# Kernel optimization log

Hardware: AMD Instinct MI355X
Metric: run time of the kernel (lower is better)

## Reference

```python
import jax, jax.numpy as jnp
import numpy as np
import math

IN_DIM = 256
HID_DIM = 256
NUM_EDGE_TYPES = 3
HEADS = 8
HEAD_DIM = HID_DIM // HEADS  # 32
QK_DIM = (NUM_EDGE_TYPES + 1) * HID_DIM  # 1024
N = 4096


def _glorot(key, shape):
    # torch_geometric-style glorot: uniform(-a, a), a = sqrt(6/(fan_in+fan_out)) over last two dims
    a = math.sqrt(6.0 / (shape[-2] + shape[-1]))
    return jax.random.uniform(key, shape, jnp.float32, -a, a)


def setup_inputs() -> dict:
    key = jax.random.key(0)
    ks = jax.random.split(key, 8)
    return {
        "input_x": jax.random.normal(ks[0], (N, IN_DIM), jnp.float32),
        "pe_Q": jax.random.normal(ks[1], (N, NUM_EDGE_TYPES * HID_DIM), jnp.float32),
        "pe_K": jax.random.normal(ks[2], (N, NUM_EDGE_TYPES * HID_DIM), jnp.float32),
        "A": jnp.zeros((N, N), jnp.int32),  # accepted by forward but unused
        "WQ": _glorot(ks[3], (HEADS, QK_DIM, HEAD_DIM)),
        "WK": _glorot(ks[4], (HEADS, QK_DIM, HEAD_DIM)),
        "WV": _glorot(ks[5], (HEADS, IN_DIM, HEAD_DIM)),
        "Q_bias": jnp.zeros((HEADS, 1, HEAD_DIM), jnp.float32),
        "K_bias": jnp.zeros((HEADS, 1, HEAD_DIM), jnp.float32),
        "V_bias": jnp.zeros((HEADS, 1, HEAD_DIM), jnp.float32),
        "lin_w": _glorot(ks[6], (HID_DIM, HID_DIM)),
        "lin_b": jnp.zeros((HID_DIM,), jnp.float32),
    }


def reference(input_x, pe_Q, pe_K, A, WQ, WK, WV, Q_bias, K_bias, V_bias, lin_w, lin_b):
    x_Q = jnp.concatenate([input_x, pe_Q], axis=-1)  # [N, QK_DIM]
    x_K = jnp.concatenate([input_x, pe_K], axis=-1)  # [N, QK_DIM]
    Q = jnp.einsum('nd,hdk->hnk', x_Q, WQ) + Q_bias   # [H, N, hd]
    K = jnp.einsum('nd,hdk->hnk', x_K, WK) + K_bias   # [H, N, hd]
    V = jnp.einsum('nd,hdk->hnk', input_x, WV) + V_bias
    scores = jnp.einsum('hnk,hmk->hnm', Q, K) / math.sqrt(HID_DIM)  # [H, N, N]
    scores = scores - jax.lax.stop_gradient(jnp.max(scores, axis=-1, keepdims=True))
    attn = jax.nn.softmax(scores, axis=-1)
    attn = jnp.where(jnp.isnan(attn), jnp.zeros_like(attn), attn)
    attn_x = jnp.einsum('hnm,hmk->hnk', attn, V)      # [H, N, hd]
    # cat(list over heads, dim=1) -> [N, H*hd] with head-major column order
    x_cat = jnp.transpose(attn_x, (1, 0, 2)).reshape(attn_x.shape[1], -1)
    return x_cat @ lin_w.T + lin_b
```

## Files before the change

### kernel.cpp

```cpp
#include <hip/hip_runtime.h>
#include <hip/hip_bf16.h>

typedef __attribute__((ext_vector_type(8))) short bf16x8;
typedef __attribute__((ext_vector_type(4))) float f32x4;

__device__ __forceinline__ unsigned short f2b(float f) {
    union { float f; unsigned int u; } v; v.f = f;
    unsigned int u = v.u;
    unsigned int r = (u + 0x7FFFu + ((u >> 16) & 1u)) >> 16;
    return (unsigned short)r;
}
__device__ __forceinline__ float b2f(unsigned short h) {
    union { unsigned int u; float f; } v; v.u = ((unsigned int)h) << 16;
    return v.f;
}
__device__ __forceinline__ unsigned pk2(float a, float b) {
    union { __hip_bfloat162 h; unsigned u; } c;
    c.h = __float22bfloat162_rn(make_float2(a, b));
    return c.u;
}


__global__ __launch_bounds__(256) void prep_w(
    const float* __restrict__ WQ, const float* __restrict__ WK,
    const float* __restrict__ WV,
    const float* __restrict__ Qb, const float* __restrict__ Kb,
    const float* __restrict__ Vb,
    unsigned short* __restrict__ WQt, unsigned short* __restrict__ WKt,
    unsigned short* __restrict__ WVt,
    unsigned short* __restrict__ Bq, unsigned short* __restrict__ Bk,
    unsigned short* __restrict__ Bv) {
    int b = blockIdx.x, t = threadIdx.x;
    if (b < 288) {
        const float* W; unsigned short* Wt; int h, d0, D; float sc = 1.0f;
        if (b < 128)      { W = WQ; Wt = WQt; h = b >> 4;   d0 = (b & 15) * 64; D = 1024; sc = 0.0625f; }
        else if (b < 256) { int bb = b - 128; W = WK; Wt = WKt; h = bb >> 4; d0 = (bb & 15) * 64; D = 1024; }
        else              { int bb = b - 256; W = WV; Wt = WVt; h = bb >> 2; d0 = (bb & 3) * 64;  D = 256; }
        __shared__ float Ts[32][65];
        int dr = t >> 2, k0 = (t & 3) * 8;
        const float* src = W + (h * D + d0 + dr) * 32 + k0;
        float4 u0 = *(const float4*)src;
        float4 u1 = *(const float4*)(src + 4);
        Ts[k0 + 0][dr] = u0.x; Ts[k0 + 1][dr] = u0.y; Ts[k0 + 2][dr] = u0.z; Ts[k0 + 3][dr] = u0.w;
        Ts[k0 + 4][dr] = u1.x; Ts[k0 + 5][dr] = u1.y; Ts[k0 + 6][dr] = u1.z; Ts[k0 + 7][dr] = u1.w;
        __syncthreads();
        int k = t >> 3, dc = (t & 7) * 8;
        union { unsigned short s[8]; uint4 v; } pk;
#pragma unroll
        for (int i = 0; i < 8; i++) pk.s[i] = f2b(Ts[k][dc + i] * sc);
        *(uint4*)(Wt + (h * 32 + k) * D + d0 + dc) = pk.v;
    } else {
        Bq[t] = f2b(Qb[t] * 0.0625f); Bk[t] = f2b(Kb[t]); Bv[t] = f2b(Vb[t]);
    }
}

__global__ __launch_bounds__(256) void proj_fused(
    const float* __restrict__ x,
    const float* __restrict__ peQ, const float* __restrict__ peK,
    const unsigned short* __restrict__ WQt, const unsigned short* __restrict__ WKt,
    const unsigned short* __restrict__ WVt,
    const unsigned short* __restrict__ Bq, const unsigned short* __restrict__ Bk,
    const unsigned short* __restrict__ Bv,
    unsigned short* __restrict__ Qc, unsigned short* __restrict__ KV) {
    __shared__ unsigned short As[64 * 72];
    __shared__ unsigned short Bs[64 * 72];
    int bx = blockIdx.x;
    int which = bx >> 8, bb = bx & 255;
    const float* A1; const unsigned short* Bt; const unsigned short* bias; int K;
    if (which == 0)      { A1 = peQ; Bt = WQt; bias = Bq; K = 1024; }
    else if (which == 1) { A1 = peK; Bt = WKt; bias = Bk; K = 1024; }
    else                 { A1 = peQ; Bt = WVt; bias = Bv; K = 256; }
    int mb = bb & 63, nb = bb >> 6;
    int m0 = mb * 64, n0 = nb * 64;
    int t = threadIdx.x, w = t >> 6, lane = t & 63;
    int ln = lane & 15, q8 = (lane >> 4) * 8;
    int wm = (w >> 1) * 32, wn = (w & 1) * 32;
    int sr = t >> 3, sc = (t & 7) * 8;
    f32x4 acc[2][2];
#pragma unroll
    for (int i = 0; i < 2; i++)
#pragma unroll
        for (int j = 0; j < 2; j++) acc[i][j] = (f32x4){0.f, 0.f, 0.f, 0.f};
    for (int kb = 0; kb < K; kb += 64) {
#pragma unroll
        for (int half = 0; half < 2; half++) {
            int r = sr + half * 32;
            int c = kb + sc;
            const float* ap = (c < 256)
                ? (x + (m0 + r) * 256 + c)
                : (A1 + (m0 + r) * 768 + (c - 256));
            float4 u0 = *(const float4*)ap;
            float4 u1 = *(const float4*)(ap + 4);
            union { unsigned u[4]; uint4 v; } pk;
            pk.u[0] = pk2(u0.x, u0.y); pk.u[1] = pk2(u0.z, u0.w);
            pk.u[2] = pk2(u1.x, u1.y); pk.u[3] = pk2(u1.z, u1.w);
            *(uint4*)&As[r * 72 + sc] = pk.v;
            *(uint4*)&Bs[r * 72 + sc] = *(const uint4*)(Bt + (n0 + r) * K + c);
        }
        __syncthreads();
#pragma unroll
        for (int ks = 0; ks < 64; ks += 32) {
            bf16x8 a[2], b[2];
#pragma unroll
            for (int i = 0; i < 2; i++) {
                a[i] = *(const bf16x8*)&As[(wm + i * 16 + ln) * 72 + ks + q8];
                b[i] = *(const bf16x8*)&Bs[(wn + i * 16 + ln) * 72 + ks + q8];
            }
#pragma unroll
            for (int i = 0; i < 2; i++)
#pragma unroll
                for (int j = 0; j < 2; j++)
                    acc[i][j] = __builtin_amdgcn_mfma_f32_16x16x32_bf16(a[i], b[j], acc[i][j], 0, 0, 0);
        }
        __syncthreads();
    }
#pragma unroll
    for (int j = 0; j < 2; j++) {
        int ncol = n0 + wn + j * 16 + ln;
        float bv = b2f(bias[ncol]);
        int h2 = ncol >> 5, din = ncol & 31;
#pragma unroll
        for (int i = 0; i < 2; i++) {
            int rbase = m0 + wm + i * 16 + ((lane >> 4) * 4);
            if (which == 0) {
#pragma unroll
                for (int r = 0; r < 4; r++)
                    Qc[(rbase + r) * 256 + ncol] = f2b(acc[i][j][r] + bv);
            } else if (which == 1) {
#pragma unroll
                for (int r = 0; r < 4; r++) {
                    int key = rbase + r;
                    int T2 = key >> 6, k6 = key & 63;
                    int kt = ((k6 >> 2) & 1) + ((k6 >> 4) & 2);
                    int ln2 = ((k6 >> 3) & 3) * 4 + (k6 & 3);
                    int addr = (h2 * 64 + T2) * 4096 + kt * 512
                             + ((din >> 3) * 16 + ln2) * 8 + (din & 7);
                    KV[addr] = f2b(acc[i][j][r] + bv);
                }
            } else {
                int key = rbase;
                int T2 = key >> 6, k6 = key & 63;
                int chunk = 4 + ((din >> 4) << 1) + ((k6 >> 5) & 1);
                int lane2 = ((k6 >> 3) & 3) * 16 + (din & 15);
                int addr = (h2 * 64 + T2) * 4096 + chunk * 512 + lane2 * 8 + (k6 & 7);
                uint2 vv;
                vv.x = pk2(acc[i][j][0] + bv, acc[i][j][1] + bv);
                vv.y = pk2(acc[i][j][2] + bv, acc[i][j][3] + bv);
                *(uint2*)(KV + addr) = vv;
            }
        }
    }
}

__global__ __launch_bounds__(256, 4) void attn_kernel(
    const unsigned short* __restrict__ Qc,
    const unsigned short* __restrict__ KV,
    unsigned short* __restrict__ Xc) {
    __shared__ float Om[4][32][33];
    __shared__ float Ls[4][32];
    int head = blockIdx.x >> 7;
    int qb = blockIdx.x & 127;
    int t = threadIdx.x, w = t >> 6, lane = t & 63;
    int ln = lane & 15, quad = lane >> 4, q8 = quad * 8;
    int q0 = qb * 32;
    bf16x8 qfv[2];
#pragma unroll
    for (int qf = 0; qf < 2; qf++)
        qfv[qf] = *(const bf16x8*)(Qc + (q0 + qf * 16 + ln) * 256 + head * 32 + q8);
    const unsigned short* kv = KV + (head * 64 + w * 16) * 4096 + lane * 8;
    f32x4 o[2][2];
#pragma unroll
    for (int qf = 0; qf < 2; qf++)
#pragma unroll
        for (int hh = 0; hh < 2; hh++) o[qf][hh] = (f32x4){0.f, 0.f, 0.f, 0.f};
    const f32x4 z = {0.f, 0.f, 0.f, 0.f};
    f32x4 lacc[2]; lacc[0] = z; lacc[1] = z;
    bf16x8 k0 = *(const bf16x8*)(kv + 0);
    bf16x8 k1 = *(const bf16x8*)(kv + 512);
    bf16x8 k2 = *(const bf16x8*)(kv + 1024);
    bf16x8 k3 = *(const bf16x8*)(kv + 1536);
    bf16x8 v0 = *(const bf16x8*)(kv + 2048);
    bf16x8 v1 = *(const bf16x8*)(kv + 2560);
    bf16x8 v2 = *(const bf16x8*)(kv + 3072);
    bf16x8 v3 = *(const bf16x8*)(kv + 3584);
#pragma unroll 1
    for (int it = 0; it < 16; it++) {
        int nit = (it < 15) ? (it + 1) : 15;
        const unsigned short* nkv = kv + nit * 4096;
        bf16x8 nk0 = *(const bf16x8*)(nkv + 0);
        bf16x8 nk1 = *(const bf16x8*)(nkv + 512);
        bf16x8 nk2 = *(const bf16x8*)(nkv + 1024);
        bf16x8 nk3 = *(const bf16x8*)(nkv + 1536);
        bf16x8 nv0 = *(const bf16x8*)(nkv + 2048);
        bf16x8 nv1 = *(const bf16x8*)(nkv + 2560);
        bf16x8 nv2 = *(const bf16x8*)(nkv + 3072);
        bf16x8 nv3 = *(const bf16x8*)(nkv + 3584);
#pragma unroll
        for (int qf = 0; qf < 2; qf++) {
            f32x4 s0 = __builtin_amdgcn_mfma_f32_16x16x32_bf16(k0, qfv[qf], z, 0, 0, 0);
            f32x4 s1 = __builtin_amdgcn_mfma_f32_16x16x32_bf16(k1, qfv[qf], z, 0, 0, 0);
            f32x4 s2 = __builtin_amdgcn_mfma_f32_16x16x32_bf16(k2, qfv[qf], z, 0, 0, 0);
            f32x4 s3 = __builtin_amdgcn_mfma_f32_16x16x32_bf16(k3, qfv[qf], z, 0, 0, 0);
            float p0[4], p1[4], p2[4], p3[4];
#pragma unroll
            for (int r = 0; r < 4; r++) {
                p0[r] = __expf(s0[r]); p1[r] = __expf(s1[r]);
                p2[r] = __expf(s2[r]); p3[r] = __expf(s3[r]);
            }
            f32x4 ps;
#pragma unroll
            for (int r = 0; r < 4; r++) ps[r] = (p0[r] + p1[r]) + (p2[r] + p3[r]);
            lacc[qf] += ps;
            union { unsigned u[4]; bf16x8 v; } b0, b1;
            b0.u[0] = pk2(p0[0], p0[1]); b0.u[1] = pk2(p0[2], p0[3]);
            b0.u[2] = pk2(p1[0], p1[1]); b0.u[3] = pk2(p1[2], p1[3]);
            b1.u[0] = pk2(p2[0], p2[1]); b1.u[1] = pk2(p2[2], p2[3]);
            b1.u[2] = pk2(p3[0], p3[1]); b1.u[3] = pk2(p3[2], p3[3]);
            o[qf][0] = __builtin_amdgcn_mfma_f32_16x16x32_bf16(v0, b0.v, o[qf][0], 0, 0, 0);
            o[qf][0] = __builtin_amdgcn_mfma_f32_16x16x32_bf16(v1, b1.v, o[qf][0], 0, 0, 0);
            o[qf][1] = __builtin_amdgcn_mfma_f32_16x16x32_bf16(v2, b0.v, o[qf][1], 0, 0, 0);
            o[qf][1] = __builtin_amdgcn_mfma_f32_16x16x32_bf16(v3, b1.v, o[qf][1], 0, 0, 0);
        }
        k0 = nk0; k1 = nk1; k2 = nk2; k3 = nk3;
        v0 = nv0; v1 = nv1; v2 = nv2; v3 = nv3;
    }
#pragma unroll
    for (int qf = 0; qf < 2; qf++) {
        float lts = (lacc[qf][0] + lacc[qf][1]) + (lacc[qf][2] + lacc[qf][3]);
        lts += __shfl_xor(lts, 16, 64);
        lts += __shfl_xor(lts, 32, 64);
#pragma unroll
        for (int r = 0; r < 4; r++) {
            Om[w][quad * 4 + r][qf * 16 + ln] = o[qf][0][r];
            Om[w][16 + quad * 4 + r][qf * 16 + ln] = o[qf][1][r];
        }
        if (quad == 0) Ls[w][qf * 16 + ln] = lts;
    }
    __syncthreads();
    int q = t & 31, d = (t >> 5) * 4;
    float num[4] = {0.f, 0.f, 0.f, 0.f};
    float den = 0.f;
#pragma unroll
    for (int w2 = 0; w2 < 4; w2++) {
        den += Ls[w2][q];
#pragma unroll
        for (int i = 0; i < 4; i++) num[i] += Om[w2][d + i][q];
    }
    float inv = 1.f / den;
    uint2 outv;
    outv.x = pk2(num[0] * inv, num[1] * inv);
    outv.y = pk2(num[2] * inv, num[3] * inv);
    *(uint2*)(Xc + (q0 + q) * 256 + head * 32 + d) = outv;
}

__global__ __launch_bounds__(256) void gemm_out(
    const unsigned short* __restrict__ A,
    const float* __restrict__ LW,
    const float* __restrict__ Lb,
    float* __restrict__ C) {
    __shared__ unsigned short As[64 * 72];
    __shared__ unsigned short Bs[64 * 72];
    int mb = blockIdx.x & 63, nb = blockIdx.x >> 6;
    int m0 = mb * 64, n0 = nb * 64;
    int t = threadIdx.x, w = t >> 6, lane = t & 63;
    int ln = lane & 15, q8 = (lane >> 4) * 8;
    int wm = (w >> 1) * 32, wn = (w & 1) * 32;
    int sr = t >> 3, sc = (t & 7) * 8;
    f32x4 acc[2][2];
#pragma unroll
    for (int i = 0; i < 2; i++)
#pragma unroll
        for (int j = 0; j < 2; j++) acc[i][j] = (f32x4){0.f, 0.f, 0.f, 0.f};
    for (int kb = 0; kb < 256; kb += 64) {
#pragma unroll
        for (int half = 0; half < 2; half++) {
            int r = sr + half * 32;
            int c = kb + sc;
            *(uint4*)&As[r * 72 + sc] = *(const uint4*)(A + (m0 + r) * 256 + c);
            const float* bp = LW + (n0 + r) * 256 + c;
            float4 u0 = *(const float4*)bp;
            float4 u1 = *(const float4*)(bp + 4);
            union { unsigned u[4]; uint4 v; } pk;
            pk.u[0] = pk2(u0.x, u0.y); pk.u[1] = pk2(u0.z, u0.w);
            pk.u[2] = pk2(u1.x, u1.y); pk.u[3] = pk2(u1.z, u1.w);
            *(uint4*)&Bs[r * 72 + sc] = pk.v;
        }
        __syncthreads();
#pragma unroll
        for (int ks = 0; ks < 64; ks += 32) {
            bf16x8 a[2], b[2];
#pragma unroll
            for (int i = 0; i < 2; i++) {
                a[i] = *(const bf16x8*)&As[(wm + i * 16 + ln) * 72 + ks + q8];
                b[i] = *(const bf16x8*)&Bs[(wn + i * 16 + ln) * 72 + ks + q8];
            }
#pragma unroll
            for (int i = 0; i < 2; i++)
#pragma unroll
                for (int j = 0; j < 2; j++)
                    acc[i][j] = __builtin_amdgcn_mfma_f32_16x16x32_bf16(a[i], b[j], acc[i][j], 0, 0, 0);
        }
        __syncthreads();
    }
#pragma unroll
    for (int j = 0; j < 2; j++) {
        int ncol = n0 + wn + j * 16 + ln;
        float bv = Lb[ncol];
#pragma unroll
        for (int i = 0; i < 2; i++) {
            int rbase = m0 + wm + i * 16 + ((lane >> 4) * 4);
#pragma unroll
            for (int r = 0; r < 4; r++)
                C[(rbase + r) * 256 + ncol] = acc[i][j][r] + bv;
        }
    }
}

extern "C" void kernel_launch(void* const* d_in, const int* in_sizes, int n_in,
                              void* d_out, int out_size, void* d_ws, size_t ws_size,
                              hipStream_t stream) {
    const float* input_x = (const float*)d_in[0];
    const float* pe_Q    = (const float*)d_in[1];
    const float* pe_K    = (const float*)d_in[2];
    const float* WQ = (const float*)d_in[4];
    const float* WK = (const float*)d_in[5];
    const float* WV = (const float*)d_in[6];
    const float* Qb = (const float*)d_in[7];
    const float* Kb = (const float*)d_in[8];
    const float* Vb = (const float*)d_in[9];
    const float* lw = (const float*)d_in[10];
    const float* lb = (const float*)d_in[11];

    unsigned short* ws = (unsigned short*)d_ws;
    unsigned short* WQt = ws;
    unsigned short* WKt = WQt + 262144;
    unsigned short* WVt = WKt + 262144;
    unsigned short* Bq  = WVt + 65536;
    unsigned short* Bk  = Bq + 256;
    unsigned short* Bv  = Bk + 256;
    unsigned short* Qc  = Bv + 256;
    unsigned short* KVb = Qc + 1048576;
    unsigned short* Xc  = KVb + 2097152;

    prep_w<<<dim3(289), dim3(256), 0, stream>>>(WQ, WK, WV, Qb, Kb, Vb,
                                                WQt, WKt, WVt, Bq, Bk, Bv);
    proj_fused<<<dim3(768), dim3(256), 0, stream>>>(input_x, pe_Q, pe_K,
                                                    WQt, WKt, WVt, Bq, Bk, Bv,
                                                    Qc, KVb);
    attn_kernel<<<dim3(1024), dim3(256), 0, stream>>>(Qc, KVb, Xc);
    gemm_out<<<dim3(256), dim3(256), 0, stream>>>(Xc, lw, lb, (float*)d_out);
}
```

Baseline: 181.9 us.

## Use 128x128 tiles for projection and output GEMMs; fold log2e into Q scale

The projection and output GEMMs move from 64x64 to 128x128 block tiles, with each wave computing a 64x64 sub-tile through a 4x4 grid of MFMA accumulators. This raises data reuse per shared-memory load but cuts the grid to 192 and 64 blocks, which leaves many of the MI355X's CUs idle. The Q scale now includes log2(e), so attention can call exp2f instead of __expf and save a multiply per score. The change risks lower occupancy and poor load balance in exchange for more arithmetic intensity per block.

```diff
diff --git a/kernel.cpp b/kernel.cpp
--- a/kernel.cpp
+++ b/kernel.cpp
@@ -1,5 +1,6 @@
 #include <hip/hip_runtime.h>
 #include <hip/hip_bf16.h>
+#include <math.h>
 
 typedef __attribute__((ext_vector_type(8))) short bf16x8;
 typedef __attribute__((ext_vector_type(4))) float f32x4;
@@ -19,6 +20,8 @@
     c.h = __float22bfloat162_rn(make_float2(a, b));
     return c.u;
 }
+
+#define QSCALE (0.0625f * 1.44269504088896f)
 
 
 __global__ __launch_bounds__(256) void prep_w(
@@ -33,7 +36,7 @@
     int b = blockIdx.x, t = threadIdx.x;
     if (b < 288) {
         const float* W; unsigned short* Wt; int h, d0, D; float sc = 1.0f;
-        if (b < 128)      { W = WQ; Wt = WQt; h = b >> 4;   d0 = (b & 15) * 64; D = 1024; sc = 0.0625f; }
+        if (b < 128)      { W = WQ; Wt = WQt; h = b >> 4;   d0 = (b & 15) * 64; D = 1024; sc = QSCALE; }
         else if (b < 256) { int bb = b - 128; W = WK; Wt = WKt; h = bb >> 4; d0 = (bb & 15) * 64; D = 1024; }
         else              { int bb = b - 256; W = WV; Wt = WVt; h = bb >> 2; d0 = (bb & 3) * 64;  D = 256; }
         __shared__ float Ts[32][65];
@@ -50,11 +53,11 @@
         for (int i = 0; i < 8; i++) pk.s[i] = f2b(Ts[k][dc + i] * sc);
         *(uint4*)(Wt + (h * 32 + k) * D + d0 + dc) = pk.v;
     } else {
-        Bq[t] = f2b(Qb[t] * 0.0625f); Bk[t] = f2b(Kb[t]); Bv[t] = f2b(Vb[t]);
-    }
-}
-
-__global__ __launch_bounds__(256) void proj_fused(
+        Bq[t] = f2b(Qb[t] * QSCALE); Bk[t] = f2b(Kb[t]); Bv[t] = f2b(Vb[t]);
+    }
+}
+
+__global__ __launch_bounds__(256) void proj128(
     const float* __restrict__ x,
     const float* __restrict__ peQ, const float* __restrict__ peK,
     const unsigned short* __restrict__ WQt, const unsigned short* __restrict__ WKt,
@@ -62,66 +65,65 @@
     const unsigned short* __restrict__ Bq, const unsigned short* __restrict__ Bk,
     const unsigned short* __restrict__ Bv,
     unsigned short* __restrict__ Qc, unsigned short* __restrict__ KV) {
-    __shared__ unsigned short As[64 * 72];
-    __shared__ unsigned short Bs[64 * 72];
+    __shared__ unsigned short As[128 * 72];
+    __shared__ unsigned short Bs[128 * 72];
     int bx = blockIdx.x;
-    int which = bx >> 8, bb = bx & 255;
+    int which = bx >> 6, bb = bx & 63;
     const float* A1; const unsigned short* Bt; const unsigned short* bias; int K;
     if (which == 0)      { A1 = peQ; Bt = WQt; bias = Bq; K = 1024; }
     else if (which == 1) { A1 = peK; Bt = WKt; bias = Bk; K = 1024; }
     else                 { A1 = peQ; Bt = WVt; bias = Bv; K = 256; }
-    int mb = bb & 63, nb = bb >> 6;
-    int m0 = mb * 64, n0 = nb * 64;
+    int mb = bb & 31, nb = bb >> 5;
+    int m0 = mb * 128, n0 = nb * 128;
     int t = threadIdx.x, w = t >> 6, lane = t & 63;
-    int ln = lane & 15, q8 = (lane >> 4) * 8;
-    int wm = (w >> 1) * 32, wn = (w & 1) * 32;
-    int sr = t >> 3, sc = (t & 7) * 8;
-    f32x4 acc[2][2];
-#pragma unroll
-    for (int i = 0; i < 2; i++)
-#pragma unroll
-        for (int j = 0; j < 2; j++) acc[i][j] = (f32x4){0.f, 0.f, 0.f, 0.f};
+    int ln = lane & 15, quad = lane >> 4, q8 = quad * 8;
+    int wm = (w >> 1) * 64, wn = (w & 1) * 64;
+    int ar = t >> 1, ac0 = (t & 1) * 32;
+    f32x4 acc[4][4];
+#pragma unroll
+    for (int i = 0; i < 4; i++)
+#pragma unroll
+        for (int j = 0; j < 4; j++) acc[i][j] = (f32x4){0.f, 0.f, 0.f, 0.f};
     for (int kb = 0; kb < K; kb += 64) {
 #pragma unroll
-        for (int half = 0; half < 2; half++) {
-            int r = sr + half * 32;
-            int c = kb + sc;
-            const float* ap = (c < 256)
-                ? (x + (m0 + r) * 256 + c)
-                : (A1 + (m0 + r) * 768 + (c - 256));
+        for (int c = 0; c < 4; c++) {
+            int col = kb + ac0 + c * 8;
+            const float* ap = (col < 256)
+                ? (x + (m0 + ar) * 256 + col)
+                : (A1 + (m0 + ar) * 768 + (col - 256));
             float4 u0 = *(const float4*)ap;
             float4 u1 = *(const float4*)(ap + 4);
             union { unsigned u[4]; uint4 v; } pk;
             pk.u[0] = pk2(u0.x, u0.y); pk.u[1] = pk2(u0.z, u0.w);
             pk.u[2] = pk2(u1.x, u1.y); pk.u[3] = pk2(u1.z, u1.w);
-            *(uint4*)&As[r * 72 + sc] = pk.v;
-            *(uint4*)&Bs[r * 72 + sc] = *(const uint4*)(Bt + (n0 + r) * K + c);
+            *(uint4*)&As[ar * 72 + ac0 + c * 8] = pk.v;
+            *(uint4*)&Bs[ar * 72 + ac0 + c * 8] = *(const uint4*)(Bt + (n0 + ar) * K + col);
         }
         __syncthreads();
 #pragma unroll
         for (int ks = 0; ks < 64; ks += 32) {
-            bf16x8 a[2], b[2];
-#pragma unroll
-            for (int i = 0; i < 2; i++) {
+            bf16x8 a[4], b[4];
+#pragma unroll
+            for (int i = 0; i < 4; i++) {
                 a[i] = *(const bf16x8*)&As[(wm + i * 16 + ln) * 72 + ks + q8];
                 b[i] = *(const bf16x8*)&Bs[(wn + i * 16 + ln) * 72 + ks + q8];
             }
 #pragma unroll
-            for (int i = 0; i < 2; i++)
-#pragma unroll
-                for (int j = 0; j < 2; j++)
+            for (int i = 0; i < 4; i++)
+#pragma unroll
+                for (int j = 0; j < 4; j++)
                     acc[i][j] = __builtin_amdgcn_mfma_f32_16x16x32_bf16(a[i], b[j], acc[i][j], 0, 0, 0);
         }
         __syncthreads();
     }
 #pragma unroll
-    for (int j = 0; j < 2; j++) {
+    for (int j = 0; j < 4; j++) {
         int ncol = n0 + wn + j * 16 + ln;
         float bv = b2f(bias[ncol]);
         int h2 = ncol >> 5, din = ncol & 31;
 #pragma unroll
-        for (int i = 0; i < 2; i++) {
-            int rbase = m0 + wm + i * 16 + ((lane >> 4) * 4);
+        for (int i = 0; i < 4; i++) {
+            int rbase = m0 + wm + i * 16 + quad * 4;
             if (which == 0) {
 #pragma unroll
                 for (int r = 0; r < 4; r++)
@@ -204,8 +206,8 @@
             float p0[4], p1[4], p2[4], p3[4];
 #pragma unroll
             for (int r = 0; r < 4; r++) {
-                p0[r] = __expf(s0[r]); p1[r] = __expf(s1[r]);
-                p2[r] = __expf(s2[r]); p3[r] = __expf(s3[r]);
+                p0[r] = exp2f(s0[r]); p1[r] = exp2f(s1[r]);
+                p2[r] = exp2f(s2[r]); p3[r] = exp2f(s3[r]);
             }
             f32x4 ps;
 #pragma unroll
@@ -253,62 +255,61 @@
     *(uint2*)(Xc + (q0 + q) * 256 + head * 32 + d) = outv;
 }
 
-__global__ __launch_bounds__(256) void gemm_out(
+__global__ __launch_bounds__(256) void out128(
     const unsigned short* __restrict__ A,
     const float* __restrict__ LW,
     const float* __restrict__ Lb,
     float* __restrict__ C) {
-    __shared__ unsigned short As[64 * 72];
-    __shared__ unsigned short Bs[64 * 72];
-    int mb = blockIdx.x & 63, nb = blockIdx.x >> 6;
-    int m0 = mb * 64, n0 = nb * 64;
+    __shared__ unsigned short As[128 * 72];
+    __shared__ unsigned short Bs[128 * 72];
+    int mb = blockIdx.x & 31, nb = blockIdx.x >> 5;
+    int m0 = mb * 128, n0 = nb * 128;
     int t = threadIdx.x, w = t >> 6, lane = t & 63;
-    int ln = lane & 15, q8 = (lane >> 4) * 8;
-    int wm = (w >> 1) * 32, wn = (w & 1) * 32;
-    int sr = t >> 3, sc = (t & 7) * 8;
-    f32x4 acc[2][2];
-#pragma unroll
-    for (int i = 0; i < 2; i++)
-#pragma unroll
-        for (int j = 0; j < 2; j++) acc[i][j] = (f32x4){0.f, 0.f, 0.f, 0.f};
+    int ln = lane & 15, quad = lane >> 4, q8 = quad * 8;
+    int wm = (w >> 1) * 64, wn = (w & 1) * 64;
+    int ar = t >> 1, ac0 = (t & 1) * 32;
+    f32x4 acc[4][4];
+#pragma unroll
+    for (int i = 0; i < 4; i++)
+#pragma unroll
+        for (int j = 0; j < 4; j++) acc[i][j] = (f32x4){0.f, 0.f, 0.f, 0.f};
     for (int kb = 0; kb < 256; kb += 64) {
 #pragma unroll
-        for (int half = 0; half < 2; half++) {
-            int r = sr + half * 32;
-            int c = kb + sc;
-            *(uint4*)&As[r * 72 + sc] = *(const uint4*)(A + (m0 + r) * 256 + c);
-            const float* bp = LW + (n0 + r) * 256 + c;
+        for (int c = 0; c < 4; c++) {
+            int col = kb + ac0 + c * 8;
+            *(uint4*)&As[ar * 72 + ac0 + c * 8] = *(const uint4*)(A + (m0 + ar) * 256 + col);
+            const float* bp = LW + (n0 + ar) * 256 + col;
             float4 u0 = *(const float4*)bp;
             float4 u1 = *(const float4*)(bp + 4);
             union { unsigned u[4]; uint4 v; } pk;
             pk.u[0] = pk2(u0.x, u0.y); pk.u[1] = pk2(u0.z, u0.w);
             pk.u[2] = pk2(u1.x, u1.y); pk.u[3] = pk2(u1.z, u1.w);
-            *(uint4*)&Bs[r * 72 + sc] = pk.v;
+            *(uint4*)&Bs[ar * 72 + ac0 + c * 8] = pk.v;
         }
         __syncthreads();
 #pragma unroll
         for (int ks = 0; ks < 64; ks += 32) {
-            bf16x8 a[2], b[2];
-#pragma unroll
-            for (int i = 0; i < 2; i++) {
+            bf16x8 a[4], b[4];
+#pragma unroll
+            for (int i = 0; i < 4; i++) {
                 a[i] = *(const bf16x8*)&As[(wm + i * 16 + ln) * 72 + ks + q8];
                 b[i] = *(const bf16x8*)&Bs[(wn + i * 16 + ln) * 72 + ks + q8];
             }
 #pragma unroll
-            for (int i = 0; i < 2; i++)
-#pragma unroll
-                for (int j = 0; j < 2; j++)
+            for (int i = 0; i < 4; i++)
+#pragma unroll
+                for (int j = 0; j < 4; j++)
                     acc[i][j] = __builtin_amdgcn_mfma_f32_16x16x32_bf16(a[i], b[j], acc[i][j], 0, 0, 0);
         }
         __syncthreads();
     }
 #pragma unroll
-    for (int j = 0; j < 2; j++) {
+    for (int j = 0; j < 4; j++) {
         int ncol = n0 + wn + j * 16 + ln;
         float bv = Lb[ncol];
 #pragma unroll
-        for (int i = 0; i < 2; i++) {
-            int rbase = m0 + wm + i * 16 + ((lane >> 4) * 4);
+        for (int i = 0; i < 4; i++) {
+            int rbase = m0 + wm + i * 16 + quad * 4;
 #pragma unroll
             for (int r = 0; r < 4; r++)
                 C[(rbase + r) * 256 + ncol] = acc[i][j][r] + bv;
@@ -344,9 +345,9 @@
 
     prep_w<<<dim3(289), dim3(256), 0, stream>>>(WQ, WK, WV, Qb, Kb, Vb,
                                                 WQt, WKt, WVt, Bq, Bk, Bv);
-    proj_fused<<<dim3(768), dim3(256), 0, stream>>>(input_x, pe_Q, pe_K,
-                                                    WQt, WKt, WVt, Bq, Bk, Bv,
-                                                    Qc, KVb);
+    proj128<<<dim3(192), dim3(256), 0, stream>>>(input_x, pe_Q, pe_K,
+                                                 WQt, WKt, WVt, Bq, Bk, Bv,
+                                                 Qc, KVb);
     attn_kernel<<<dim3(1024), dim3(256), 0, stream>>>(Qc, KVb, Xc);
-    gemm_out<<<dim3(256), dim3(256), 0, stream>>>(Xc, lw, lb, (float*)d_out);
-}
+    out128<<<dim3(64), dim3(256), 0, stream>>>(Xc, lw, lb, (float*)d_out);
+}
```

After: 222.0 us. 1.22x slower.

## Fuse all stages into one persistent cooperative kernel with grid syncs

Applied to the files above, without the earlier changes.

Merges the weight prep, projection, attention and output GEMM kernels into a single cooperative persistent kernel. Stages are separated by grid.sync(), and blocks loop over the virtual block indices of each stage. The aim is to remove the launch gaps between the four kernels. The trade-offs are the grid-wide barrier cost, a grid capped by occupancy (256 CUs times blocks per CU), register pressure from inlining every stage into one function, and slower time slicing on stages that were previously launched wider. A fallback path keeps the separate launches if the occupancy query fails.

```diff
diff --git a/kernel.cpp b/kernel.cpp
--- a/kernel.cpp
+++ b/kernel.cpp
@@ -1,5 +1,8 @@
 #include <hip/hip_runtime.h>
+#include <hip/hip_cooperative_groups.h>
 #include <hip/hip_bf16.h>
+
+namespace cg = cooperative_groups;
 
 typedef __attribute__((ext_vector_type(8))) short bf16x8;
 typedef __attribute__((ext_vector_type(4))) float f32x4;
@@ -20,8 +23,13 @@
     return c.u;
 }
 
-
-__global__ __launch_bounds__(256) void prep_w(
+struct SMemGemm { unsigned short As[64 * 72]; unsigned short Bs[64 * 72]; };
+struct SMemAttn { float Om[4][32][33]; float Ls[4][32]; };
+struct SMemPrep { float Ts[32][65]; };
+union SMemU { SMemGemm g; SMemAttn a; SMemPrep p; };
+
+
+__device__ __forceinline__ void prep_body(int b, SMemU& sm,
     const float* __restrict__ WQ, const float* __restrict__ WK,
     const float* __restrict__ WV,
     const float* __restrict__ Qb, const float* __restrict__ Kb,
@@ -30,31 +38,33 @@
     unsigned short* __restrict__ WVt,
     unsigned short* __restrict__ Bq, unsigned short* __restrict__ Bk,
     unsigned short* __restrict__ Bv) {
-    int b = blockIdx.x, t = threadIdx.x;
+    int t = threadIdx.x;
     if (b < 288) {
         const float* W; unsigned short* Wt; int h, d0, D; float sc = 1.0f;
         if (b < 128)      { W = WQ; Wt = WQt; h = b >> 4;   d0 = (b & 15) * 64; D = 1024; sc = 0.0625f; }
         else if (b < 256) { int bb = b - 128; W = WK; Wt = WKt; h = bb >> 4; d0 = (bb & 15) * 64; D = 1024; }
         else              { int bb = b - 256; W = WV; Wt = WVt; h = bb >> 2; d0 = (bb & 3) * 64;  D = 256; }
-        __shared__ float Ts[32][65];
         int dr = t >> 2, k0 = (t & 3) * 8;
         const float* src = W + (h * D + d0 + dr) * 32 + k0;
         float4 u0 = *(const float4*)src;
         float4 u1 = *(const float4*)(src + 4);
-        Ts[k0 + 0][dr] = u0.x; Ts[k0 + 1][dr] = u0.y; Ts[k0 + 2][dr] = u0.z; Ts[k0 + 3][dr] = u0.w;
-        Ts[k0 + 4][dr] = u1.x; Ts[k0 + 5][dr] = u1.y; Ts[k0 + 6][dr] = u1.z; Ts[k0 + 7][dr] = u1.w;
+        sm.p.Ts[k0 + 0][dr] = u0.x; sm.p.Ts[k0 + 1][dr] = u0.y;
+        sm.p.Ts[k0 + 2][dr] = u0.z; sm.p.Ts[k0 + 3][dr] = u0.w;
+        sm.p.Ts[k0 + 4][dr] = u1.x; sm.p.Ts[k0 + 5][dr] = u1.y;
+        sm.p.Ts[k0 + 6][dr] = u1.z; sm.p.Ts[k0 + 7][dr] = u1.w;
         __syncthreads();
         int k = t >> 3, dc = (t & 7) * 8;
         union { unsigned short s[8]; uint4 v; } pk;
 #pragma unroll
-        for (int i = 0; i < 8; i++) pk.s[i] = f2b(Ts[k][dc + i] * sc);
+        for (int i = 0; i < 8; i++) pk.s[i] = f2b(sm.p.Ts[k][dc + i] * sc);
         *(uint4*)(Wt + (h * 32 + k) * D + d0 + dc) = pk.v;
     } else {
         Bq[t] = f2b(Qb[t] * 0.0625f); Bk[t] = f2b(Kb[t]); Bv[t] = f2b(Vb[t]);
     }
-}
-
-__global__ __launch_bounds__(256) void proj_fused(
+    __syncthreads();
+}
+
+__device__ __forceinline__ void proj_body(int bx, SMemU& sm,
     const float* __restrict__ x,
     const float* __restrict__ peQ, const float* __restrict__ peK,
     const unsigned short* __restrict__ WQt, const unsigned short* __restrict__ WKt,
@@ -62,9 +72,6 @@
     const unsigned short* __restrict__ Bq, const unsigned short* __restrict__ Bk,
     const unsigned short* __restrict__ Bv,
     unsigned short* __restrict__ Qc, unsigned short* __restrict__ KV) {
-    __shared__ unsigned short As[64 * 72];
-    __shared__ unsigned short Bs[64 * 72];
-    int bx = blockIdx.x;
     int which = bx >> 8, bb = bx & 255;
     const float* A1; const unsigned short* Bt; const unsigned short* bias; int K;
     if (which == 0)      { A1 = peQ; Bt = WQt; bias = Bq; K = 1024; }
@@ -94,8 +101,8 @@
             union { unsigned u[4]; uint4 v; } pk;
             pk.u[0] = pk2(u0.x, u0.y); pk.u[1] = pk2(u0.z, u0.w);
             pk.u[2] = pk2(u1.x, u1.y); pk.u[3] = pk2(u1.z, u1.w);
-            *(uint4*)&As[r * 72 + sc] = pk.v;
-            *(uint4*)&Bs[r * 72 + sc] = *(const uint4*)(Bt + (n0 + r) * K + c);
+            *(uint4*)&sm.g.As[r * 72 + sc] = pk.v;
+            *(uint4*)&sm.g.Bs[r * 72 + sc] = *(const uint4*)(Bt + (n0 + r) * K + c);
         }
         __syncthreads();
 #pragma unroll
@@ -103,8 +110,8 @@
             bf16x8 a[2], b[2];
 #pragma unroll
             for (int i = 0; i < 2; i++) {
-                a[i] = *(const bf16x8*)&As[(wm + i * 16 + ln) * 72 + ks + q8];
-                b[i] = *(const bf16x8*)&Bs[(wn + i * 16 + ln) * 72 + ks + q8];
+                a[i] = *(const bf16x8*)&sm.g.As[(wm + i * 16 + ln) * 72 + ks + q8];
+                b[i] = *(const bf16x8*)&sm.g.Bs[(wn + i * 16 + ln) * 72 + ks + q8];
             }
 #pragma unroll
             for (int i = 0; i < 2; i++)
@@ -150,16 +157,15 @@
             }
         }
     }
-}
-
-__global__ __launch_bounds__(256, 4) void attn_kernel(
+    __syncthreads();
+}
+
+__device__ __forceinline__ void attn_body(int bid, SMemU& sm,
     const unsigned short* __restrict__ Qc,
     const unsigned short* __restrict__ KV,
     unsigned short* __restrict__ Xc) {
-    __shared__ float Om[4][32][33];
-    __shared__ float Ls[4][32];
-    int head = blockIdx.x >> 7;
-    int qb = blockIdx.x & 127;
+    int head = bid >> 7;
+    int qb = bid & 127;
     int t = threadIdx.x, w = t >> 6, lane = t & 63;
     int ln = lane & 15, quad = lane >> 4, q8 = quad * 8;
     int q0 = qb * 32;
@@ -231,10 +237,10 @@
         lts += __shfl_xor(lts, 32, 64);
 #pragma unroll
         for (int r = 0; r < 4; r++) {
-            Om[w][quad * 4 + r][qf * 16 + ln] = o[qf][0][r];
-            Om[w][16 + quad * 4 + r][qf * 16 + ln] = o[qf][1][r];
-        }
-        if (quad == 0) Ls[w][qf * 16 + ln] = lts;
+            sm.a.Om[w][quad * 4 + r][qf * 16 + ln] = o[qf][0][r];
+            sm.a.Om[w][16 + quad * 4 + r][qf * 16 + ln] = o[qf][1][r];
+        }
+        if (quad == 0) sm.a.Ls[w][qf * 16 + ln] = lts;
     }
     __syncthreads();
     int q = t & 31, d = (t >> 5) * 4;
@@ -242,25 +248,24 @@
     float den = 0.f;
 #pragma unroll
     for (int w2 = 0; w2 < 4; w2++) {
-        den += Ls[w2][q];
-#pragma unroll
-        for (int i = 0; i < 4; i++) num[i] += Om[w2][d + i][q];
+        den += sm.a.Ls[w2][q];
+#pragma unroll
+        for (int i = 0; i < 4; i++) num[i] += sm.a.Om[w2][d + i][q];
     }
     float inv = 1.f / den;
     uint2 outv;
     outv.x = pk2(num[0] * inv, num[1] * inv);
     outv.y = pk2(num[2] * inv, num[3] * inv);
     *(uint2*)(Xc + (q0 + q) * 256 + head * 32 + d) = outv;
-}
-
-__global__ __launch_bounds__(256) void gemm_out(
+    __syncthreads();
+}
+
+__device__ __forceinline__ void out_body(int bid, SMemU& sm,
     const unsigned short* __restrict__ A,
     const float* __restrict__ LW,
     const float* __restrict__ Lb,
     float* __restrict__ C) {
-    __shared__ unsigned short As[64 * 72];
-    __shared__ unsigned short Bs[64 * 72];
-    int mb = blockIdx.x & 63, nb = blockIdx.x >> 6;
+    int mb = bid & 63, nb = bid >> 6;
     int m0 = mb * 64, n0 = nb * 64;
     int t = threadIdx.x, w = t >> 6, lane = t & 63;
     int ln = lane & 15, q8 = (lane >> 4) * 8;
@@ -276,14 +281,14 @@
         for (int half = 0; half < 2; half++) {
             int r = sr + half * 32;
             int c = kb + sc;
-            *(uint4*)&As[r * 72 + sc] = *(const uint4*)(A + (m0 + r) * 256 + c);
+            *(uint4*)&sm.g.As[r * 72 + sc] = *(const uint4*)(A + (m0 + r) * 256 + c);
             const float* bp = LW + (n0 + r) * 256 + c;
             float4 u0 = *(const float4*)bp;
             float4 u1 = *(const float4*)(bp + 4);
             union { unsigned u[4]; uint4 v; } pk;
             pk.u[0] = pk2(u0.x, u0.y); pk.u[1] = pk2(u0.z, u0.w);
             pk.u[2] = pk2(u1.x, u1.y); pk.u[3] = pk2(u1.z, u1.w);
-            *(uint4*)&Bs[r * 72 + sc] = pk.v;
+            *(uint4*)&sm.g.Bs[r * 72 + sc] = pk.v;
         }
         __syncthreads();
 #pragma unroll
@@ -291,8 +296,8 @@
             bf16x8 a[2], b[2];
 #pragma unroll
             for (int i = 0; i < 2; i++) {
-                a[i] = *(const bf16x8*)&As[(wm + i * 16 + ln) * 72 + ks + q8];
-                b[i] = *(const bf16x8*)&Bs[(wn + i * 16 + ln) * 72 + ks + q8];
+                a[i] = *(const bf16x8*)&sm.g.As[(wm + i * 16 + ln) * 72 + ks + q8];
+                b[i] = *(const bf16x8*)&sm.g.Bs[(wn + i * 16 + ln) * 72 + ks + q8];
             }
 #pragma unroll
             for (int i = 0; i < 2; i++)
@@ -314,6 +319,59 @@
                 C[(rbase + r) * 256 + ncol] = acc[i][j][r] + bv;
         }
     }
+    __syncthreads();
+}
+
+__global__ __launch_bounds__(256, 4) void mega(
+    const float* x, const float* peQ, const float* peK,
+    const float* WQ, const float* WK, const float* WV,
+    const float* Qb, const float* Kb, const float* Vb,
+    const float* LW, const float* Lb,
+    unsigned short* WQt, unsigned short* WKt, unsigned short* WVt,
+    unsigned short* Bq, unsigned short* Bk, unsigned short* Bv,
+    unsigned short* Qc, unsigned short* KV, unsigned short* Xc,
+    float* out) {
+    __shared__ SMemU sm;
+    cg::grid_group grid = cg::this_grid();
+    int G = gridDim.x, bid = blockIdx.x;
+    for (int vb = bid; vb < 289; vb += G)
+        prep_body(vb, sm, WQ, WK, WV, Qb, Kb, Vb, WQt, WKt, WVt, Bq, Bk, Bv);
+    grid.sync();
+    for (int vb = bid; vb < 768; vb += G)
+        proj_body(vb, sm, x, peQ, peK, WQt, WKt, WVt, Bq, Bk, Bv, Qc, KV);
+    grid.sync();
+    for (int vb = bid; vb < 1024; vb += G)
+        attn_body(vb, sm, Qc, KV, Xc);
+    grid.sync();
+    for (int vb = bid; vb < 256; vb += G)
+        out_body(vb, sm, Xc, LW, Lb, out);
+}
+
+__global__ __launch_bounds__(256) void k_prep(
+    const float* WQ, const float* WK, const float* WV,
+    const float* Qb, const float* Kb, const float* Vb,
+    unsigned short* WQt, unsigned short* WKt, unsigned short* WVt,
+    unsigned short* Bq, unsigned short* Bk, unsigned short* Bv) {
+    __shared__ SMemU sm;
+    prep_body(blockIdx.x, sm, WQ, WK, WV, Qb, Kb, Vb, WQt, WKt, WVt, Bq, Bk, Bv);
+}
+__global__ __launch_bounds__(256) void k_proj(
+    const float* x, const float* peQ, const float* peK,
+    const unsigned short* WQt, const unsigned short* WKt, const unsigned short* WVt,
+    const unsigned short* Bq, const unsigned short* Bk, const unsigned short* Bv,
+    unsigned short* Qc, unsigned short* KV) {
+    __shared__ SMemU sm;
+    proj_body(blockIdx.x, sm, x, peQ, peK, WQt, WKt, WVt, Bq, Bk, Bv, Qc, KV);
+}
+__global__ __launch_bounds__(256, 4) void k_attn(
+    const unsigned short* Qc, const unsigned short* KV, unsigned short* Xc) {
+    __shared__ SMemU sm;
+    attn_body(blockIdx.x, sm, Qc, KV, Xc);
+}
+__global__ __launch_bounds__(256) void k_out(
+    const unsigned short* A, const float* LW, const float* Lb, float* C) {
+    __shared__ SMemU sm;
+    out_body(blockIdx.x, sm, A, LW, Lb, C);
 }
 
 extern "C" void kernel_launch(void* const* d_in, const int* in_sizes, int n_in,
@@ -341,12 +399,30 @@
     unsigned short* Qc  = Bv + 256;
     unsigned short* KVb = Qc + 1048576;
     unsigned short* Xc  = KVb + 2097152;
-
-    prep_w<<<dim3(289), dim3(256), 0, stream>>>(WQ, WK, WV, Qb, Kb, Vb,
-                                                WQt, WKt, WVt, Bq, Bk, Bv);
-    proj_fused<<<dim3(768), dim3(256), 0, stream>>>(input_x, pe_Q, pe_K,
+    float* outp = (float*)d_out;
+
+    int maxb = 0;
+    hipError_t occ = hipOccupancyMaxActiveBlocksPerMultiprocessor(&maxb, mega, 256, 0);
+    if (occ == hipSuccess && maxb >= 1) {
+        int grid = maxb * 256; if (grid > 1024) grid = 1024;
+        void* args[] = {
+            (void*)&input_x, (void*)&pe_Q, (void*)&pe_K,
+            (void*)&WQ, (void*)&WK, (void*)&WV,
+            (void*)&Qb, (void*)&Kb, (void*)&Vb,
+            (void*)&lw, (void*)&lb,
+            (void*)&WQt, (void*)&WKt, (void*)&WVt,
+            (void*)&Bq, (void*)&Bk, (void*)&Bv,
+            (void*)&Qc, (void*)&KVb, (void*)&Xc,
+            (void*)&outp };
+        hipLaunchCooperativeKernel((const void*)mega, dim3(grid), dim3(256),
+                                   args, 0, stream);
+    } else {
+        k_prep<<<dim3(289), dim3(256), 0, stream>>>(WQ, WK, WV, Qb, Kb, Vb,
+                                                    WQt, WKt, WVt, Bq, Bk, Bv);
+        k_proj<<<dim3(768), dim3(256), 0, stream>>>(input_x, pe_Q, pe_K,
                                                     WQt, WKt, WVt, Bq, Bk, Bv,
                                                     Qc, KVb);
-    attn_kernel<<<dim3(1024), dim3(256), 0, stream>>>(Qc, KVb, Xc);
-    gemm_out<<<dim3(256), dim3(256), 0, stream>>>(Xc, lw, lb, (float*)d_out);
-}
+        k_attn<<<dim3(1024), dim3(256), 0, stream>>>(Qc, KVb, Xc);
+        k_out<<<dim3(256), dim3(256), 0, stream>>>(Xc, lw, lb, outp);
+    }
+}
```

New measurement: 378.2 us. 2.08x slower.
